# Optimization experiments

Hardware: AMD Instinct MI355X
Metric: run time of the kernel (lower is better)

Reference implementation:

```python
import jax, jax.numpy as jnp
import numpy as np

B, S, D, H = 2, 2048, 1024, 16
DK = D // H


def setup_inputs() -> dict:
    key = jax.random.key(0)
    ks = jax.random.split(key, 12)
    s = 1.0 / np.sqrt(D)
    inp = {
        "query": jax.random.normal(ks[0], (B, S, D), jnp.float32),
        "key_": jax.random.normal(ks[1], (B, S, D), jnp.float32),
        "value": jax.random.normal(ks[2], (B, S, D), jnp.float32),
        # causal mask, broadcast over heads: [B, 1, S, S]
        "mask": jnp.broadcast_to(jnp.tril(jnp.ones((S, S), bool)), (B, 1, S, S)),
        "W_q": jax.random.uniform(ks[3], (D, D), jnp.float32, -s, s),
        "b_q": jax.random.uniform(ks[4], (D,), jnp.float32, -s, s),
        "W_k": jax.random.uniform(ks[5], (D, D), jnp.float32, -s, s),
        "b_k": jax.random.uniform(ks[6], (D,), jnp.float32, -s, s),
        "W_v": jax.random.uniform(ks[7], (D, D), jnp.float32, -s, s),
        "b_v": jax.random.uniform(ks[8], (D,), jnp.float32, -s, s),
        "W_o": jax.random.uniform(ks[9], (D, D), jnp.float32, -s, s),
        "b_o": jax.random.uniform(ks[10], (D,), jnp.float32, -s, s),
    }
    return inp


def reference(query, key_, value, mask, W_q, b_q, W_k, b_k, W_v, b_v, W_o, b_o):
    b = query.shape[0]
    # linear projections (torch Linear: x @ W.T + b)
    Q = query @ W_q.T + b_q
    K = key_ @ W_k.T + b_k
    V = value @ W_v.T + b_v
    # [b, S, H, dk] -> [b, H, S, dk]
    Q = Q.reshape(b, -1, H, DK).transpose(0, 2, 1, 3)
    K = K.reshape(b, -1, H, DK).transpose(0, 2, 1, 3)
    V = V.reshape(b, -1, H, DK).transpose(0, 2, 1, 3)
    scores = jnp.einsum("bhqd,bhkd->bhqk", Q, K) / jnp.sqrt(jnp.float32(DK))
    scores = jnp.where(mask, scores, -jnp.inf)
    attn = jax.nn.softmax(scores, axis=-1)
    out = jnp.einsum("bhqk,bhkd->bhqd", attn, V)
    out = out.transpose(0, 2, 1, 3).reshape(b, -1, D)
    return out @ W_o.T + b_o
```

## Files before the change

kernel.cpp:

```cpp
#include <hip/hip_runtime.h>
#include <hip/hip_bf16.h>
#include <stdint.h>

#define B_ 2
#define S_ 2048
#define D_ 1024
#define H_ 16
#define DK_ 64

typedef __attribute__((ext_vector_type(4))) float floatx4;
typedef __attribute__((ext_vector_type(8))) short shortx8;
typedef __attribute__((ext_vector_type(4))) short shortx4;
typedef unsigned short ushort_t;

__device__ inline ushort_t f2bf(float f) {
  union { float f; unsigned u; } v; v.f = f;
  unsigned r = v.u + 0x7FFFu + ((v.u >> 16) & 1u);
  return (ushort_t)(r >> 16);
}

__device__ inline unsigned pack2bf(float lo, float hi) {
  return __builtin_amdgcn_perm(__float_as_uint(hi), __float_as_uint(lo), 0x07060302u);
}

__device__ inline shortx4 mk_sx4(unsigned lo, unsigned hi) {
  union { unsigned u[2]; shortx4 s; } v; v.u[0] = lo; v.u[1] = hi; return v.s;
}

__device__ inline float fast_exp2(float x) {
#if __has_builtin(__builtin_amdgcn_exp2f)
  return __builtin_amdgcn_exp2f(x);
#else
  return __expf(0.69314718056f * x);
#endif
}

__device__ inline void gload_lds16(const void* g, void* l) {
  __builtin_amdgcn_global_load_lds(
      (const __attribute__((address_space(1))) unsigned int*)g,
      (__attribute__((address_space(3))) unsigned int*)l, 16, 0, 0);
}

__device__ inline floatx4 mfma16x16x16bf16(shortx4 a, shortx4 b, floatx4 c) {
#if __has_builtin(__builtin_amdgcn_mfma_f32_16x16x16bf16_1k)
  return __builtin_amdgcn_mfma_f32_16x16x16bf16_1k(a, b, c, 0, 0, 0);
#else
  floatx4 d;
  asm("v_mfma_f32_16x16x16_bf16 %0, %1, %2, %3" : "=v"(d) : "v"(a), "v"(b), "v"(c));
  return d;
#endif
}

struct ConvArgs {
  const float* src[7];
  ushort_t* dst[7];
};

__global__ __launch_bounds__(256) void convert_kernel(ConvArgs a) {
  int blk = blockIdx.x;
  int seg, bis;
  if (blk < 3072) { seg = blk >> 10; bis = blk & 1023; }
  else { int bb = blk - 3072; seg = 3 + (bb >> 8); bis = bb & 255; }
  const float4* src = (const float4*)(a.src[seg]) + (size_t)bis * 1024;
  ushort4* dst = (ushort4*)(a.dst[seg]) + (size_t)bis * 1024;
#pragma unroll
  for (int i = 0; i < 4; ++i) {
    int idx = i * 256 + threadIdx.x;
    float4 v = src[idx];
    ushort4 o;
    o.x = f2bf(v.x); o.y = f2bf(v.y); o.z = f2bf(v.z); o.w = f2bf(v.w);
    dst[idx] = o;
  }
}

template <int TM>
__device__ inline void gemm_bt_core(const ushort_t* __restrict__ A,
                                    const ushort_t* __restrict__ W,
                                    const float* __restrict__ bias,
                                    float scl,
                                    void* __restrict__ outp,
                                    int m0, int n0, int N, int K, int outmode) {
  constexpr int LDSU = (TM + 128) * 32;
  constexpr int GA = TM / 16;
  constexpr int GW = (GA + 8) / 4;
  constexpr int MI = TM / 32;
  __shared__ ushort_t smem[2][LDSU];
  const int tid = threadIdx.x;
  const int wave = tid >> 6;
  const int lane = tid & 63;
  const int quad = lane >> 4;
  const int l16 = lane & 15;
  const int wm = (wave >> 1) * (TM / 2);
  const int wn = (wave & 1) * 64;

  floatx4 acc[MI][4] = {};

  const ushort_t* gsrc[GW];
  int ldst[GW];
#pragma unroll
  for (int i = 0; i < GW; ++i) {
    int g = wave * GW + i;
    int row = lane >> 2;
    int col = (lane & 3) * 8;
    if (g < GA) {
      gsrc[i] = A + (size_t)(m0 + g * 16 + row) * K + col;
      ldst[i] = g * 512;
    } else {
      gsrc[i] = W + (size_t)(n0 + (g - GA) * 16 + row) * K + col;
      ldst[i] = TM * 32 + (g - GA) * 512;
    }
  }

#pragma unroll
  for (int i = 0; i < GW; ++i) gload_lds16(gsrc[i], &smem[0][ldst[i]]);

  const int niter = K >> 5;
  for (int j = 0; j < niter; ++j) {
    __syncthreads();
    if (j + 1 < niter) {
      const int ko = (j + 1) * 32;
      ushort_t* bufn = smem[(j + 1) & 1];
#pragma unroll
      for (int i = 0; i < GW; ++i) gload_lds16(gsrc[i] + ko, bufn + ldst[i]);
    }
    const ushort_t* aT = smem[j & 1];
    const ushort_t* bT = smem[j & 1] + TM * 32;
    shortx8 af[MI], bf[4];
#pragma unroll
    for (int mi = 0; mi < MI; ++mi)
      af[mi] = *(const shortx8*)(aT + (wm + mi * 16 + l16) * 32 + quad * 8);
#pragma unroll
    for (int ni = 0; ni < 4; ++ni)
      bf[ni] = *(const shortx8*)(bT + (wn + ni * 16 + l16) * 32 + quad * 8);
#pragma unroll
    for (int mi = 0; mi < MI; ++mi)
#pragma unroll
      for (int ni = 0; ni < 4; ++ni)
        acc[mi][ni] = __builtin_amdgcn_mfma_f32_16x16x32_bf16(af[mi], bf[ni], acc[mi][ni], 0, 0, 0);
  }

#pragma unroll
  for (int ni = 0; ni < 4; ++ni) {
    int n = n0 + wn + ni * 16 + l16;
    float bv = bias[n];
#pragma unroll
    for (int mi = 0; mi < MI; ++mi) {
      if (outmode == 2) {
        int m = m0 + wm + mi * 16 + quad * 4;
        int b = m >> 11, s = m & 2047;
        ushort_t* dst = (ushort_t*)outp + (((size_t)(b * 1024 + n)) << 11) + s;
        uint2 pk;
        pk.x = (unsigned)f2bf(acc[mi][ni][0] + bv) |
               ((unsigned)f2bf(acc[mi][ni][1] + bv) << 16);
        pk.y = (unsigned)f2bf(acc[mi][ni][2] + bv) |
               ((unsigned)f2bf(acc[mi][ni][3] + bv) << 16);
        *(uint2*)(dst) = pk;
      } else {
#pragma unroll
        for (int r = 0; r < 4; ++r) {
          int m = m0 + wm + mi * 16 + quad * 4 + r;
          float v = (acc[mi][ni][r] + bv) * scl;
          if (outmode == 1) ((float*)outp)[(size_t)m * N + n] = v;
          else ((ushort_t*)outp)[(size_t)m * N + n] = f2bf(v);
        }
      }
    }
  }
}

struct QkvArgs {
  const ushort_t* A[3];
  const ushort_t* W[3];
  const float* bias[3];
  ushort_t* out[3];
  float scale[3];
};

__global__ __launch_bounds__(256) void gemm_qkv_kernel(QkvArgs a) {
  int z = blockIdx.z;
  int m0 = (blockIdx.x * 4 + (blockIdx.y >> 3)) * 128;
  int n0 = (blockIdx.y & 7) * 128;
  gemm_bt_core<128>(a.A[z], a.W[z], a.bias[z], a.scale[z], a.out[z],
                    m0, n0, D_, D_, z == 2 ? 2 : 0);
}

__global__ __launch_bounds__(256) void gemm_out_kernel(const ushort_t* __restrict__ A,
                                                       const ushort_t* __restrict__ W,
                                                       const float* __restrict__ bias,
                                                       float* __restrict__ out) {
  int m0 = (blockIdx.x * 8 + (blockIdx.y >> 3)) * 64;
  int n0 = (blockIdx.y & 7) * 128;
  gemm_bt_core<64>(A, W, bias, 1.0f, out, m0, n0, D_, D_, 1);
}

__global__ __launch_bounds__(256, 2) void attn_kernel(const ushort_t* __restrict__ Qp,
                                                      const ushort_t* __restrict__ Kp,
                                                      const ushort_t* __restrict__ Vt,
                                                      ushort_t* __restrict__ O) {
  const int id = blockIdx.x;
  const int h = id & 15;
  const int qq = (id & 255) >> 4;
  const int b = id >> 8;
  const int qt = b ? qq : 15 - qq;
  const int q0 = qt * 128;
  const int tid = threadIdx.x;
  const int wave = tid >> 6;
  const int lane = tid & 63;
  const int quad = lane >> 4;
  const int l16 = lane & 15;

  __shared__ ushort_t smem[2][16384];

  const size_t hoff = (size_t)h * DK_;

  shortx8 qf[2][2];
#pragma unroll
  for (int grp = 0; grp < 2; ++grp) {
    const ushort_t* qrow = Qp + ((size_t)b * S_ + q0 + wave * 32 + grp * 16 + l16) * D_ + hoff;
#pragma unroll
    for (int ks = 0; ks < 2; ++ks)
      qf[grp][ks] = *(const shortx8*)(qrow + ks * 32 + quad * 8);
  }

  const int r8 = lane >> 3;
  const int jj8 = ((lane & 7) ^ r8) * 8;
  const ushort_t* kb[4];
#pragma unroll
  for (int g = 0; g < 4; ++g) {
    int r = wave * 32 + g * 8 + r8;
    kb[g] = Kp + ((size_t)b * S_ + r) * D_ + hoff + jj8;
  }
  const int r4 = lane >> 4;
  const ushort_t* vb[4];
#pragma unroll
  for (int g = 0; g < 4; ++g) {
    int r = wave * 16 + g * 4 + r4;
    int cpos = ((lane & 15) ^ ((g * 4 + r4) & 15)) * 8;
    vb[g] = Vt + ((size_t)(b * H_ + h) * 64 + r) * S_ + cpos;
  }

  floatx4 oacc[2][4] = {};
  float l_run[2] = {0.f, 0.f};
  const int nj = qt + 1;
  const int qwave_max = q0 + wave * 32 + 31;

#pragma unroll
  for (int g = 0; g < 4; ++g) {
    gload_lds16(kb[g], &smem[0][wave * 2048 + g * 512]);
    gload_lds16(vb[g], &smem[0][8192 + wave * 2048 + g * 512]);
  }

  for (int j = 0; j < nj; ++j) {
    __syncthreads();
    if (j + 1 < nj) {
      ushort_t* bufn = smem[(j + 1) & 1];
      const size_t ko = (size_t)(j + 1) * 128 * D_;
      const int vo = (j + 1) * 128;
#pragma unroll
      for (int g = 0; g < 4; ++g) {
        gload_lds16(kb[g] + ko, bufn + wave * 2048 + g * 512);
        gload_lds16(vb[g] + vo, bufn + 8192 + wave * 2048 + g * 512);
      }
    }
    if (j * 128 > qwave_max) continue;
    const ushort_t* k_lds = smem[j & 1];
    const ushort_t* v_lds = smem[j & 1] + 8192;

#pragma unroll
    for (int half = 0; half < 2; ++half) {
      const int kbase = j * 128 + half * 64;
      if (kbase > qwave_max) break;

      floatx4 sacc[2][4];
#pragma unroll
      for (int kkb = 0; kkb < 4; ++kkb) {
        const ushort_t* krow = k_lds + (half * 64 + kkb * 16 + l16) * 64;
        shortx8 af0 = *(const shortx8*)(krow + (quad ^ (l16 & 7)) * 8);
        shortx8 af1 = *(const shortx8*)(krow + ((4 | quad) ^ (l16 & 7)) * 8);
#pragma unroll
        for (int grp = 0; grp < 2; ++grp) {
          floatx4 acc = {0.f, 0.f, 0.f, 0.f};
          acc = __builtin_amdgcn_mfma_f32_16x16x32_bf16(af0, qf[grp][0], acc, 0, 0, 0);
          acc = __builtin_amdgcn_mfma_f32_16x16x32_bf16(af1, qf[grp][1], acc, 0, 0, 0);
          sacc[grp][kkb] = acc;
        }
      }
#pragma unroll
      for (int grp = 0; grp < 2; ++grp) {
        const int qg = q0 + wave * 32 + grp * 16 + l16;
        if (kbase + 63 > q0 + wave * 32 + grp * 16) {
#pragma unroll
          for (int kkb = 0; kkb < 4; ++kkb)
#pragma unroll
            for (int r = 0; r < 4; ++r)
              if (kbase + kkb * 16 + quad * 4 + r > qg) sacc[grp][kkb][r] = -3.0e38f;
        }
      }

      shortx4 pf[2][4];
#pragma unroll
      for (int grp = 0; grp < 2; ++grp) {
        float psum = 0.f;
#pragma unroll
        for (int kkb = 0; kkb < 4; ++kkb) {
          float p0 = fast_exp2(sacc[grp][kkb][0]);
          float p1 = fast_exp2(sacc[grp][kkb][1]);
          float p2 = fast_exp2(sacc[grp][kkb][2]);
          float p3 = fast_exp2(sacc[grp][kkb][3]);
          psum += (p0 + p1) + (p2 + p3);
          pf[grp][kkb] = mk_sx4(pack2bf(p0, p1), pack2bf(p2, p3));
        }
        l_run[grp] += psum;
      }

#pragma unroll
      for (int kkb = 0; kkb < 4; ++kkb) {
        const int jj = ((half * 8 + kkb * 2 + (quad >> 1)) ^ l16) * 8 + (quad & 1) * 4;
#pragma unroll
        for (int db = 0; db < 4; ++db) {
          shortx4 vf = *(const shortx4*)(v_lds + (db * 16 + l16) * 128 + jj);
          oacc[0][db] = mfma16x16x16bf16(vf, pf[0][kkb], oacc[0][db]);
          oacc[1][db] = mfma16x16x16bf16(vf, pf[1][kkb], oacc[1][db]);
        }
      }
    }
  }

  __syncthreads();
  ushort_t* sm = &smem[0][0];
#pragma unroll
  for (int grp = 0; grp < 2; ++grp) {
    float l0 = l_run[grp];
    l0 += __shfl_xor(l0, 16);
    l0 += __shfl_xor(l0, 32);
    float inv_l = 1.0f / l0;
    int row = wave * 32 + grp * 16 + l16;
#pragma unroll
    for (int db = 0; db < 4; ++db) {
#pragma unroll
      for (int rr = 0; rr < 2; ++rr) {
        unsigned pk = pack2bf(oacc[grp][db][rr * 2] * inv_l, oacc[grp][db][rr * 2 + 1] * inv_l);
        *(unsigned*)(sm + row * 72 + db * 16 + quad * 4 + rr * 2) = pk;
      }
    }
  }
  __syncthreads();
  {
    int r = tid >> 1, c = (tid & 1) * 32;
    const ushort_t* src = sm + r * 72 + c;
    ushort_t* dst = O + ((size_t)b * S_ + q0 + r) * D_ + hoff + c;
    uint4 v0 = *(const uint4*)(src);
    uint4 v1 = *(const uint4*)(src + 8);
    uint4 v2 = *(const uint4*)(src + 16);
    uint4 v3 = *(const uint4*)(src + 24);
    *(uint4*)(dst) = v0;
    *(uint4*)(dst + 8) = v1;
    *(uint4*)(dst + 16) = v2;
    *(uint4*)(dst + 24) = v3;
  }
}

extern "C" void kernel_launch(void* const* d_in, const int* in_sizes, int n_in,
                              void* d_out, int out_size, void* d_ws, size_t ws_size,
                              hipStream_t stream) {
  (void)in_sizes; (void)n_in; (void)out_size; (void)ws_size;
  char* ws = (char*)d_ws;
  ushort_t* xq = (ushort_t*)(ws + 0);
  ushort_t* xk = (ushort_t*)(ws + 8388608);
  ushort_t* xv = (ushort_t*)(ws + 16777216);
  ushort_t* wq = (ushort_t*)(ws + 25165824);
  ushort_t* wk = (ushort_t*)(ws + 27262976);
  ushort_t* wv = (ushort_t*)(ws + 29360128);
  ushort_t* wo = (ushort_t*)(ws + 31457280);
  ushort_t* Qp = (ushort_t*)(ws + 33554432);
  ushort_t* Kp = (ushort_t*)(ws + 41943040);
  ushort_t* Vt = (ushort_t*)(ws + 50331648);
  ushort_t* O = xq;

  ConvArgs ca;
  ca.src[0] = (const float*)d_in[0];  ca.dst[0] = xq;
  ca.src[1] = (const float*)d_in[1];  ca.dst[1] = xk;
  ca.src[2] = (const float*)d_in[2];  ca.dst[2] = xv;
  ca.src[3] = (const float*)d_in[4];  ca.dst[3] = wq;
  ca.src[4] = (const float*)d_in[6];  ca.dst[4] = wk;
  ca.src[5] = (const float*)d_in[8];  ca.dst[5] = wv;
  ca.src[6] = (const float*)d_in[10]; ca.dst[6] = wo;
  convert_kernel<<<dim3(4096), dim3(256), 0, stream>>>(ca);

  QkvArgs qa;
  qa.A[0] = xq; qa.W[0] = wq; qa.bias[0] = (const float*)d_in[5]; qa.out[0] = Qp;
  qa.A[1] = xk; qa.W[1] = wk; qa.bias[1] = (const float*)d_in[7]; qa.out[1] = Kp;
  qa.A[2] = xv; qa.W[2] = wv; qa.bias[2] = (const float*)d_in[9]; qa.out[2] = Vt;
  qa.scale[0] = 0.125f * 1.44269504089f;
  qa.scale[1] = 1.0f;
  qa.scale[2] = 1.0f;
  gemm_qkv_kernel<<<dim3(8, 32, 3), dim3(256), 0, stream>>>(qa);

  attn_kernel<<<dim3(512), dim3(256), 0, stream>>>(Qp, Kp, Vt, O);

  gemm_out_kernel<<<dim3(8, 64, 1), dim3(256), 0, stream>>>(
      O, wo, (const float*)d_in[11], (float*)d_out);
}
```

Before: 224.5 us.

## Replace QKV projection GEMM with 256x256-tile pipelined 8-wave kernel

Swaps the 128x128-tile QKV GEMM for a new 512-thread kernel that computes 256x256 output tiles. It double-buffers 64-wide K slices in LDS with direct global-to-LDS loads, and staggers loads across four barrier-separated phases interleaved with 16x16x32 bf16 MFMA groups under raised wave priority. The aim is more data reuse per tile and overlap of memory traffic with matrix math. The cost is fewer blocks (192), 128KB of LDS per block, heavy register use, and hand-tuned vmcnt waits that must match the exact load ordering.

```diff
diff --git a/kernel.cpp b/kernel.cpp
--- a/kernel.cpp
+++ b/kernel.cpp
@@ -49,6 +49,12 @@
   asm("v_mfma_f32_16x16x16_bf16 %0, %1, %2, %3" : "=v"(d) : "v"(a), "v"(b), "v"(c));
   return d;
 #endif
+}
+
+__device__ inline void bar() {
+  asm volatile("" ::: "memory");
+  __builtin_amdgcn_s_barrier();
+  asm volatile("" ::: "memory");
 }
 
 struct ConvArgs {
@@ -176,12 +182,163 @@
   float scale[3];
 };
 
-__global__ __launch_bounds__(256) void gemm_qkv_kernel(QkvArgs a) {
-  int z = blockIdx.z;
-  int m0 = (blockIdx.x * 4 + (blockIdx.y >> 3)) * 128;
-  int n0 = (blockIdx.y & 7) * 128;
-  gemm_bt_core<128>(a.A[z], a.W[z], a.bias[z], a.scale[z], a.out[z],
-                    m0, n0, D_, D_, z == 2 ? 2 : 0);
+#define NTK 16
+
+#define STG_A(h, i, t, bufofs) \
+  gload_lds16(srcA2[h] + (size_t)(i) * 8192 + (size_t)(t) * 64, smemf + (bufofs) + ldsA0[h] + (i) * 512)
+#define STG_B(h, i, t, bufofs) \
+  gload_lds16(srcB2[h] + (size_t)(i) * 8192 + (size_t)(t) * 64, smemf + (bufofs) + ldsB0[h] + (i) * 512)
+
+#define RD_A(AS, bufofs, mibase)                                                        \
+  {                                                                                     \
+    _Pragma("unroll") for (int i_ = 0; i_ < 2; ++i_) {                                  \
+      AS[i_][0] = *(const shortx8*)(aBase + (bufofs) + ((mibase) + i_) * 1024 + coff[0]); \
+      AS[i_][1] = *(const shortx8*)(aBase + (bufofs) + ((mibase) + i_) * 1024 + coff[1]); \
+    }                                                                                   \
+  }
+
+#define RD_B(BS, bufofs)                                                                \
+  {                                                                                     \
+    _Pragma("unroll") for (int ni_ = 0; ni_ < 4; ++ni_) {                               \
+      BS[ni_][0] = *(const shortx8*)(bBase + (bufofs) + ni_ * 1024 + coff[0]);          \
+      BS[ni_][1] = *(const shortx8*)(bBase + (bufofs) + ni_ * 1024 + coff[1]);          \
+    }                                                                                   \
+  }
+
+#define MFMA_PH(AS, BR, MIB)                                                            \
+  {                                                                                     \
+    __builtin_amdgcn_s_setprio(1);                                                      \
+    _Pragma("unroll") for (int i_ = 0; i_ < 2; ++i_) {                                  \
+      _Pragma("unroll") for (int ni_ = 0; ni_ < 4; ++ni_) {                             \
+        acc[(MIB) + i_][ni_] = __builtin_amdgcn_mfma_f32_16x16x32_bf16(                 \
+            AS[i_][0], BR[ni_][0], acc[(MIB) + i_][ni_], 0, 0, 0);                      \
+        acc[(MIB) + i_][ni_] = __builtin_amdgcn_mfma_f32_16x16x32_bf16(                 \
+            AS[i_][1], BR[ni_][1], acc[(MIB) + i_][ni_], 0, 0, 0);                      \
+      }                                                                                 \
+    }                                                                                   \
+    __builtin_amdgcn_s_setprio(0);                                                      \
+  }
+
+#define TILE(T, BC, BO, BRD, BWR)                                                       \
+  {                                                                                     \
+                \
+    RD_A(as0, BC, 2);                                                                   \
+    if ((T) + 1 < NTK) { STG_A(1, 0, (T) + 1, BO); STG_A(1, 1, (T) + 1, BO); }          \
+    bar();                                                                              \
+    MFMA_PH(as1, BRD, 0);                                                               \
+    bar();                                                                              \
+                         \
+    RD_A(as1, BC, 4);                                                                   \
+    if ((T) + 2 < NTK) { STG_B(0, 0, (T) + 2, BC); STG_B(0, 1, (T) + 2, BC); }          \
+    bar();                                                                              \
+    MFMA_PH(as0, BRD, 2);                                                               \
+    bar();                                                                              \
+                                       \
+    RD_A(as0, BC, 6);                                                                   \
+    if ((T) + 2 < NTK) { STG_B(1, 0, (T) + 2, BC); STG_B(1, 1, (T) + 2, BC); }          \
+    bar();                                                                              \
+    MFMA_PH(as1, BRD, 4);                                                               \
+    bar();                                                                              \
+         \
+    if ((T) + 2 < NTK) {                                                                \
+      STG_A(0, 0, (T) + 2, BC); STG_A(0, 1, (T) + 2, BC);                               \
+      asm volatile("s_waitcnt vmcnt(6)" ::: "memory");                                  \
+    } else if ((T) + 1 < NTK) {                                                         \
+      asm volatile("s_waitcnt vmcnt(0)" ::: "memory");                                  \
+    }                                                                                   \
+    bar();                                                                              \
+    if ((T) + 1 < NTK) { RD_B(BWR, BO); RD_A(as1, BO, 0); }                             \
+    MFMA_PH(as0, BRD, 6);                                                               \
+    bar();                                                                              \
+  }
+
+__global__ __launch_bounds__(512) void gemm_qkv256_kernel(QkvArgs a) {
+  const int z = blockIdx.z;
+  const ushort_t* __restrict__ A = a.A[z];
+  const ushort_t* __restrict__ W = a.W[z];
+  const float* __restrict__ bias = a.bias[z];
+  const float scl = a.scale[z];
+  ushort_t* __restrict__ outp = a.out[z];
+  const int outmode = (z == 2) ? 2 : 0;
+  const int m0 = blockIdx.x * 256;
+  const int n0 = blockIdx.y * 256;
+
+  __shared__ ushort_t smem[2][32768];
+  ushort_t* smemf = &smem[0][0];
+
+  const int tid = threadIdx.x;
+  const int wave = tid >> 6;
+  const int lane = tid & 63;
+  const int quad = lane >> 4;
+  const int l16 = lane & 15;
+  const int wm = wave >> 2;
+  const int wnl = (wave & 3) * 64;
+
+  const int grow = lane >> 3;
+  const int gchunk = ((lane & 7) ^ grow) * 8;
+  const ushort_t* srcA2[2];
+  const ushort_t* srcB2[2];
+  int ldsA0[2], ldsB0[2];
+#pragma unroll
+  for (int h = 0; h < 2; ++h) {
+    srcA2[h] = A + (size_t)(m0 + h * 128 + wave * 16 + grow) * 1024 + gchunk;
+    srcB2[h] = W + (size_t)(n0 + h * 128 + wave * 16 + grow) * 1024 + gchunk;
+    ldsA0[h] = (h * 128 + wave * 16) * 64;
+    ldsB0[h] = 16384 + (h * 128 + wave * 16) * 64;
+  }
+
+  int coff[2];
+  coff[0] = (quad ^ (l16 & 7)) * 8;
+  coff[1] = ((4 | quad) ^ (l16 & 7)) * 8;
+  const ushort_t* aBase = smemf + (wm * 128 + l16) * 64;
+  const ushort_t* bBase = smemf + 16384 + (wnl + l16) * 64;
+
+  floatx4 acc[8][4] = {};
+  shortx8 as0[2][2], as1[2][2];
+  shortx8 bA[4][2], bB[4][2];
+
+  STG_B(0, 0, 0, 0); STG_B(0, 1, 0, 0);
+  STG_B(1, 0, 0, 0); STG_B(1, 1, 0, 0);
+  STG_A(0, 0, 0, 0); STG_A(0, 1, 0, 0);
+  STG_A(1, 0, 0, 0); STG_A(1, 1, 0, 0);
+  STG_B(0, 0, 1, 32768); STG_B(0, 1, 1, 32768);
+  STG_B(1, 0, 1, 32768); STG_B(1, 1, 1, 32768);
+  STG_A(0, 0, 1, 32768); STG_A(0, 1, 1, 32768);
+  asm volatile("s_waitcnt vmcnt(6)" ::: "memory");
+  bar();
+  RD_B(bA, 0);
+  RD_A(as1, 0, 0);
+
+  for (int t = 0; t < NTK; t += 2) {
+    TILE(t, 0, 32768, bA, bB);
+    TILE(t + 1, 32768, 0, bB, bA);
+  }
+
+#pragma unroll
+  for (int ni = 0; ni < 4; ++ni) {
+    const int n = n0 + wnl + ni * 16 + l16;
+    const float bv = bias[n];
+#pragma unroll
+    for (int mi = 0; mi < 8; ++mi) {
+      if (outmode == 2) {
+        int m = m0 + wm * 128 + mi * 16 + quad * 4;
+        int b = m >> 11, s = m & 2047;
+        ushort_t* dst = outp + (((size_t)(b * 1024 + n)) << 11) + s;
+        uint2 pk;
+        pk.x = (unsigned)f2bf(acc[mi][ni][0] + bv) |
+               ((unsigned)f2bf(acc[mi][ni][1] + bv) << 16);
+        pk.y = (unsigned)f2bf(acc[mi][ni][2] + bv) |
+               ((unsigned)f2bf(acc[mi][ni][3] + bv) << 16);
+        *(uint2*)(dst) = pk;
+      } else {
+#pragma unroll
+        for (int r = 0; r < 4; ++r) {
+          int m = m0 + wm * 128 + mi * 16 + quad * 4 + r;
+          outp[(size_t)m * 1024 + n] = f2bf((acc[mi][ni][r] + bv) * scl);
+        }
+      }
+    }
+  }
 }
 
 __global__ __launch_bounds__(256) void gemm_out_kernel(const ushort_t* __restrict__ A,
@@ -394,7 +551,7 @@
   qa.scale[0] = 0.125f * 1.44269504089f;
   qa.scale[1] = 1.0f;
   qa.scale[2] = 1.0f;
-  gemm_qkv_kernel<<<dim3(8, 32, 3), dim3(256), 0, stream>>>(qa);
+  gemm_qkv256_kernel<<<dim3(16, 4, 3), dim3(512), 0, stream>>>(qa);
 
   attn_kernel<<<dim3(512), dim3(256), 0, stream>>>(Qp, Kp, Vt, O);
 
```

Measured after the change: 278.8 us. +24.2%, slower.
